# Kernel optimization log

Measured on AMD Instinct MI355X. Metric: run time of the kernel, lower is better.

## Reference

```python
import jax, jax.numpy as jnp
import numpy as np

N = 4096
IN_DIM = 256
OUT_DIM = 256
H = 4
D = OUT_DIM // H  # per-head dim (concat=True)
ALPHA = 0.2
NEG_INF = -9e15


def setup_inputs() -> dict:
    key = jax.random.key(0)
    k1, k2, k3, k4, k5 = jax.random.split(key, 5)
    h = jax.random.normal(k1, (N, IN_DIM), dtype=jnp.float32)
    adj = jax.random.randint(k2, (N, N), 0, 2, dtype=jnp.int32)
    # Linear params (torch Linear: y = x @ W.T + b), xavier_uniform gain=1.414
    lim_w = 1.414 * np.sqrt(6.0 / (IN_DIM + H * D))
    W = jax.random.uniform(k3, (H * D, IN_DIM), dtype=jnp.float32, minval=-lim_w, maxval=lim_w)
    b = jnp.zeros((H * D,), dtype=jnp.float32)
    lim_a = 1.414 * np.sqrt(6.0 / (H + 2 * D))
    a = jax.random.uniform(k4, (H, 2 * D), dtype=jnp.float32, minval=-lim_a, maxval=lim_a)
    return {"h": h, "adj": adj, "W": W, "b": b, "a": a}


def reference(h, adj, W, b, a):
    # Wh: [N, H, D]
    Wh = (h @ W.T + b).reshape(N, H, D)
    # e_ij = leakyrelu(a . [Wh_i ; Wh_j]) decomposed into src/dst parts
    src = jnp.einsum('nhd,hd->nh', Wh, a[:, :D])   # [N, H], contribution of node i
    dst = jnp.einsum('nhd,hd->nh', Wh, a[:, D:])   # [N, H], contribution of node j
    e = src[:, None, :] + dst[None, :, :]          # [N, N, H]
    e = jax.nn.leaky_relu(e, negative_slope=ALPHA)
    # dense mask: non-edges get -9e15 (matches the original fill)
    att = jnp.where(adj[:, :, None] == 1, e, NEG_INF)
    att = jax.nn.softmax(att, axis=1)              # softmax over neighbors j per row i
    # dropout skipped (eval mode / deterministic reference)
    h_prime = jnp.einsum('ijh,jhd->ihd', att, Wh)  # [N, H, D]
    return h_prime.reshape(N, H * D)               # concat=True
```

## Files before the change

### kernel.cpp

```cpp
#include <hip/hip_runtime.h>

#define NN 4096
#define ALPHA 0.2f
#define FLTMAX 3.402823466e+38f

typedef __attribute__((ext_vector_type(8))) short short8x;
typedef __attribute__((ext_vector_type(4))) float f32x4;
typedef __attribute__((ext_vector_type(4))) unsigned short ushort4x;
typedef unsigned long long u64;

__device__ __forceinline__ float lrelu(float x) { return x > 0.f ? x : ALPHA * x; }

__device__ __forceinline__ unsigned short f2bf(float f) {
  unsigned u = __float_as_uint(f);
  u += 0x7fffu + ((u >> 16) & 1u);
  return (unsigned short)(u >> 16);
}
__device__ __forceinline__ float bf2f(unsigned short s) {
  return __uint_as_float(((unsigned)s) << 16);
}
__device__ __forceinline__ unsigned fkey(float f) {
  unsigned b = __float_as_uint(f);
  return (b & 0x80000000u) ? ~b : (b | 0x80000000u);
}
__device__ __forceinline__ float funkey(unsigned k) {
  return __uint_as_float((k & 0x80000000u) ? (k & 0x7fffffffu) : ~k);
}

__global__ __launch_bounds__(256) void k0_prep(
    const float* __restrict__ W, unsigned short* __restrict__ Whi,
    unsigned short* __restrict__ Wlo, unsigned* __restrict__ dmaxkey)
{
  const int t = threadIdx.x;
  const int idx = blockIdx.x * 256 + t;
  float4 v = ((const float4*)W)[idx];
  const float vf[4] = {v.x, v.y, v.z, v.w};
  ushort4x hi, lo;
#pragma unroll
  for (int q = 0; q < 4; ++q) {
    unsigned short hb = f2bf(vf[q]);
    hi[q] = hb;
    lo[q] = f2bf(vf[q] - bf2f(hb));
  }
  ((ushort4x*)Whi)[idx] = hi;
  ((ushort4x*)Wlo)[idx] = lo;
  if (blockIdx.x == 0 && t < 4) dmaxkey[t] = 0x00800000u;
}

__global__ __launch_bounds__(256) void k1_mfma(
    const float* __restrict__ hin, const unsigned short* __restrict__ Whi,
    const unsigned short* __restrict__ Wlo, const float* __restrict__ bias,
    const float* __restrict__ av, unsigned short* __restrict__ WhT,
    float* __restrict__ srcv, float* __restrict__ dstv_soa,
    unsigned* __restrict__ dmaxkey)
{
  __shared__ float lds_s[4][16], lds_d[4][16];
  const int t = threadIdx.x;
  const int rb = blockIdx.x >> 2, h = blockIdx.x & 3;
  const int m0 = rb * 16;
  const int w = t >> 6, l = t & 63, r = l & 15, g = l >> 4;
  const int d = w * 16 + r;
  const int col = h * 64 + d;

  f32x4 acc = (f32x4){0.f, 0.f, 0.f, 0.f};
  const float* arow = hin + (size_t)(m0 + r) * 256 + g * 8;
  const unsigned short* bh = Whi + (size_t)col * 256 + g * 8;
  const unsigned short* bl = Wlo + (size_t)col * 256 + g * 8;

#pragma unroll
  for (int ks = 0; ks < 8; ++ks) {
    float4 a0 = *(const float4*)(arow + ks * 32);
    float4 a1 = *(const float4*)(arow + ks * 32 + 4);
    const float af[8] = {a0.x, a0.y, a0.z, a0.w, a1.x, a1.y, a1.z, a1.w};
    short8x ahi, alo;
#pragma unroll
    for (int j = 0; j < 8; ++j) {
      unsigned short hb = f2bf(af[j]);
      ahi[j] = (short)hb;
      alo[j] = (short)f2bf(af[j] - bf2f(hb));
    }
    short8x bhf = *(const short8x*)(bh + ks * 32);
    short8x blf = *(const short8x*)(bl + ks * 32);
    acc = __builtin_amdgcn_mfma_f32_16x16x32_bf16(ahi, bhf, acc, 0, 0, 0);
    acc = __builtin_amdgcn_mfma_f32_16x16x32_bf16(ahi, blf, acc, 0, 0, 0);
    acc = __builtin_amdgcn_mfma_f32_16x16x32_bf16(alo, bhf, acc, 0, 0, 0);
  }

  const float bc = bias[col];
  const float asrc = av[h * 128 + d];
  const float adst = av[h * 128 + 64 + d];
  float wv[4];
  ushort4x st;
#pragma unroll
  for (int q = 0; q < 4; ++q) {
    wv[q] = acc[q] + bc;
    st[q] = f2bf(wv[q]);
  }
  *(ushort4x*)(WhT + (size_t)col * NN + m0 + 4 * g) = st;

#pragma unroll
  for (int q = 0; q < 4; ++q) {
    float s = wv[q] * asrc, dd = wv[q] * adst;
#pragma unroll
    for (int off = 8; off >= 1; off >>= 1) {
      s += __shfl_xor(s, off);
      dd += __shfl_xor(dd, off);
    }
    if (r == 0) { lds_s[w][4 * g + q] = s; lds_d[w][4 * g + q] = dd; }
  }
  __syncthreads();
  if (t < 64) {
    const int row = t & 15;
    float s = lds_s[0][row] + lds_s[1][row] + lds_s[2][row] + lds_s[3][row];
    float dd = lds_d[0][row] + lds_d[1][row] + lds_d[2][row] + lds_d[3][row];
    if (t < 16) {
      srcv[(size_t)(m0 + row) * 4 + h] = s;
      dstv_soa[(size_t)h * NN + m0 + row] = dd;
    }
    float m = dd;
#pragma unroll
    for (int off = 1; off <= 32; off <<= 1) m = fmaxf(m, __shfl_xor(m, off));
    if (t == 0) atomicMax(dmaxkey + h, fkey(m));
  }
}

__global__ __launch_bounds__(256) void k2_mask(
    const int* __restrict__ adj, u64* __restrict__ bmask)
{
  const int t = threadIdx.x, wid = t >> 6, l = t & 63;
  const int row = blockIdx.x * 4 + wid;
  const int4* ap = (const int4*)(adj + (size_t)row * NN) + l;
  const int sh = 4 * (l & 15);
#pragma unroll
  for (int it = 0; it < 16; ++it) {
    int4 v = ap[(size_t)it * 64];
    unsigned nib = (v.x & 1) | ((v.y & 1) << 1) | ((v.z & 1) << 2) | ((v.w & 1) << 3);
    u64 w = (u64)nib << sh;
    w |= __shfl_xor(w, 1);
    w |= __shfl_xor(w, 2);
    w |= __shfl_xor(w, 4);
    w |= __shfl_xor(w, 8);
    if ((l & 15) == 0) bmask[(size_t)row * 64 + it * 4 + (l >> 4)] = w;
  }
}

__global__ __launch_bounds__(256) void k3_mfma(
    const unsigned short* __restrict__ WhT, const float* __restrict__ srcv,
    const float* __restrict__ dstv_soa, const unsigned* __restrict__ dmaxkey,
    const u64* __restrict__ bmask,
    float* __restrict__ pacc, float* __restrict__ pden)
{
  const int t = threadIdx.x;
  const int rb = blockIdx.x & 255, s = blockIdx.x >> 8;
  const int i0 = rb * 16;
  const int w0 = s * 16;
  const int h  = t >> 6;
  const int l  = t & 63;
  const int r  = l & 15;
  const int g  = l >> 4;

  const float dmax = funkey(dmaxkey[h]);
  const float sr0 = srcv[(size_t)(i0 + r) * 4 + h];
  const float mr0 = lrelu(sr0 + dmax);

  f32x4 acc[4];
#pragma unroll
  for (int n = 0; n < 4; ++n) acc[n] = (f32x4){0.f, 0.f, 0.f, 0.f};
  float dacc0 = 0.f;

  const unsigned short* whb = WhT + (size_t)(h * 64 + r) * NN + s * 1024 + g * 8;
  const float* dpb = dstv_soa + (size_t)h * NN + s * 1024 + g * 8;
  const u64* mb0 = bmask + (size_t)(i0 + r) * 64 + w0;

  for (int tile = 0; tile < 16; ++tile) {
    const u64 wm0 = mb0[tile];
#pragma unroll
    for (int kt = 0; kt < 2; ++kt) {
      float4 da = *(const float4*)(dpb + tile * 64 + kt * 32);
      float4 db = *(const float4*)(dpb + tile * 64 + kt * 32 + 4);
      const unsigned bits0 = (unsigned)(wm0 >> (kt * 32 + g * 8)) & 0xffu;
      const float dvs[8] = {da.x, da.y, da.z, da.w, db.x, db.y, db.z, db.w};
      short8x a0;
#pragma unroll
      for (int jj = 0; jj < 8; ++jj) {
        float e0 = lrelu(sr0 + dvs[jj]);
        float p0 = ((bits0 >> jj) & 1u) ? __expf(e0 - mr0) : 0.f;
        unsigned short pb0 = f2bf(p0);
        a0[jj] = (short)pb0;
        dacc0 += bf2f(pb0);
      }
      short8x bfr[4];
#pragma unroll
      for (int n = 0; n < 4; ++n)
        bfr[n] = *(const short8x*)(whb + (size_t)(n * 16) * NN + tile * 64 + kt * 32);
#pragma unroll
      for (int n = 0; n < 4; ++n)
        acc[n] = __builtin_amdgcn_mfma_f32_16x16x32_bf16(a0, bfr[n], acc[n], 0, 0, 0);
    }
  }

  dacc0 += __shfl_xor(dacc0, 16); dacc0 += __shfl_xor(dacc0, 32);
  if (l < 16) pden[((size_t)s * NN + i0 + l) * 4 + h] = dacc0;

#pragma unroll
  for (int n = 0; n < 4; ++n)
#pragma unroll
    for (int q = 0; q < 4; ++q)
      pacc[((size_t)s * NN + i0 + g * 4 + q) * 256 + h * 64 + n * 16 + r] = acc[n][q];
}

__global__ __launch_bounds__(256) void k4_combine(
    const float* __restrict__ pacc, const float* __restrict__ pden,
    float* __restrict__ out)
{
  const int t = threadIdx.x;
  const int i = blockIdx.x * 4 + (t >> 6);
  const int c4 = t & 63;
  const int h = c4 >> 4;
  const float4* pa = (const float4*)pacc;
  float4 num = {0.f, 0.f, 0.f, 0.f};
  float den = 0.f;
#pragma unroll
  for (int s = 0; s < 4; ++s) {
    float4 v = pa[((size_t)(s * NN + i)) * 64 + c4];
    num.x += v.x; num.y += v.y; num.z += v.z; num.w += v.w;
    den += pden[((size_t)s * NN + i) * 4 + h];
  }
  float inv = 1.f / den;
  float4 o = {num.x * inv, num.y * inv, num.z * inv, num.w * inv};
  ((float4*)out)[(size_t)i * 64 + c4] = o;
}

extern "C" void kernel_launch(void* const* d_in, const int* in_sizes, int n_in,
                              void* d_out, int out_size, void* d_ws, size_t ws_size,
                              hipStream_t stream) {
  const float* hin  = (const float*)d_in[0];
  const int*   adj  = (const int*)d_in[1];
  const float* W    = (const float*)d_in[2];
  const float* bias = (const float*)d_in[3];
  const float* av   = (const float*)d_in[4];
  float* out = (float*)d_out;

  char* ws = (char*)d_ws;
  unsigned short* WhT = (unsigned short*)(ws + 0x0);
  unsigned short* Whi = (unsigned short*)(ws + 0x200000);
  unsigned short* Wlo = (unsigned short*)(ws + 0x220000);
  float* srcv  = (float*)(ws + 0x240000);
  float* dstv  = (float*)(ws + 0x250000);
  unsigned* dmaxkey = (unsigned*)(ws + 0x260000);
  u64* bmask   = (u64*)(ws + 0x261000);
  float* pacc  = (float*)(ws + 0x461000);
  float* pden  = (float*)(ws + 0x1461000);

  k0_prep<<<64, 256, 0, stream>>>(W, Whi, Wlo, dmaxkey);
  k1_mfma<<<1024, 256, 0, stream>>>(hin, Whi, Wlo, bias, av, WhT, srcv, dstv, dmaxkey);
  k2_mask<<<1024, 256, 0, stream>>>(adj, bmask);
  k3_mfma<<<1024, 256, 0, stream>>>(WhT, srcv, dstv, dmaxkey, bmask, pacc, pden);
  k4_combine<<<NN / 4, 256, 0, stream>>>(pacc, pden, out);
}
```

Before: 212.4 us.

## Process two row tiles per wave sharing B fragments, split K across waves, use exp2

```diff
diff --git a/kernel.cpp b/kernel.cpp
--- a/kernel.cpp
+++ b/kernel.cpp
@@ -3,13 +3,12 @@
 #define NN 4096
 #define ALPHA 0.2f
 #define FLTMAX 3.402823466e+38f
+#define LOG2E 1.44269504088896340736f
 
 typedef __attribute__((ext_vector_type(8))) short short8x;
 typedef __attribute__((ext_vector_type(4))) float f32x4;
 typedef __attribute__((ext_vector_type(4))) unsigned short ushort4x;
 typedef unsigned long long u64;
-
-__device__ __forceinline__ float lrelu(float x) { return x > 0.f ? x : ALPHA * x; }
 
 __device__ __forceinline__ unsigned short f2bf(float f) {
   unsigned u = __float_as_uint(f);
@@ -106,7 +105,7 @@
       s += __shfl_xor(s, off);
       dd += __shfl_xor(dd, off);
     }
-    if (r == 0) { lds_s[w][4 * g + q] = s; lds_d[w][4 * g + q] = dd; }
+    if (r == 0) { lds_s[w][4 * g + q] = s * LOG2E; lds_d[w][4 * g + q] = dd * LOG2E; }
   }
   __syncthreads();
   if (t < 64) {
@@ -144,69 +143,118 @@
   }
 }
 
-__global__ __launch_bounds__(256) void k3_mfma(
+__global__ __launch_bounds__(256, 4) void k3_mfma(
     const unsigned short* __restrict__ WhT, const float* __restrict__ srcv,
     const float* __restrict__ dstv_soa, const unsigned* __restrict__ dmaxkey,
     const u64* __restrict__ bmask,
     float* __restrict__ pacc, float* __restrict__ pden)
 {
+  __shared__ float lds_acc[2][64][33];
+  __shared__ float lds_den[2][64][2];
   const int t = threadIdx.x;
-  const int rb = blockIdx.x & 255, s = blockIdx.x >> 8;
-  const int i0 = rb * 16;
-  const int w0 = s * 16;
-  const int h  = t >> 6;
-  const int l  = t & 63;
-  const int r  = l & 15;
-  const int g  = l >> 4;
+  const int c  = blockIdx.x & 7;
+  const int s  = c >> 1, hp = c & 1;
+  const int rb = blockIdx.x >> 3;
+  const int i0 = rb * 32;
+  const int w = t >> 6, l = t & 63;
+  const int hsel = w & 1, jh = w >> 1;
+  const int h = hp * 2 + hsel;
+  const int r = l & 15, g = l >> 4;
+  const int j0 = s * 1024 + jh * 512;
 
   const float dmax = funkey(dmaxkey[h]);
   const float sr0 = srcv[(size_t)(i0 + r) * 4 + h];
-  const float mr0 = lrelu(sr0 + dmax);
-
-  f32x4 acc[4];
-#pragma unroll
-  for (int n = 0; n < 4; ++n) acc[n] = (f32x4){0.f, 0.f, 0.f, 0.f};
-  float dacc0 = 0.f;
-
-  const unsigned short* whb = WhT + (size_t)(h * 64 + r) * NN + s * 1024 + g * 8;
-  const float* dpb = dstv_soa + (size_t)h * NN + s * 1024 + g * 8;
-  const u64* mb0 = bmask + (size_t)(i0 + r) * 64 + w0;
-
-  for (int tile = 0; tile < 16; ++tile) {
+  const float sr1 = srcv[(size_t)(i0 + 16 + r) * 4 + h];
+  const float x0m = sr0 + dmax, x1m = sr1 + dmax;
+  const float mr0 = fmaxf(x0m, ALPHA * x0m);
+  const float mr1 = fmaxf(x1m, ALPHA * x1m);
+
+  f32x4 acc[2][4];
+#pragma unroll
+  for (int m = 0; m < 2; ++m)
+#pragma unroll
+    for (int n = 0; n < 4; ++n) acc[m][n] = (f32x4){0.f, 0.f, 0.f, 0.f};
+  float dacc0 = 0.f, dacc1 = 0.f;
+
+  const unsigned short* whb = WhT + (size_t)(h * 64 + r) * NN + j0 + g * 8;
+  const float* dpb = dstv_soa + (size_t)h * NN + j0 + g * 8;
+  const u64* mb0 = bmask + (size_t)(i0 + r) * 64 + s * 16 + jh * 8;
+  const u64* mb1 = bmask + (size_t)(i0 + 16 + r) * 64 + s * 16 + jh * 8;
+
+  for (int tile = 0; tile < 8; ++tile) {
     const u64 wm0 = mb0[tile];
+    const u64 wm1 = mb1[tile];
 #pragma unroll
     for (int kt = 0; kt < 2; ++kt) {
       float4 da = *(const float4*)(dpb + tile * 64 + kt * 32);
       float4 db = *(const float4*)(dpb + tile * 64 + kt * 32 + 4);
       const unsigned bits0 = (unsigned)(wm0 >> (kt * 32 + g * 8)) & 0xffu;
+      const unsigned bits1 = (unsigned)(wm1 >> (kt * 32 + g * 8)) & 0xffu;
       const float dvs[8] = {da.x, da.y, da.z, da.w, db.x, db.y, db.z, db.w};
-      short8x a0;
+      short8x a0, a1;
 #pragma unroll
       for (int jj = 0; jj < 8; ++jj) {
-        float e0 = lrelu(sr0 + dvs[jj]);
-        float p0 = ((bits0 >> jj) & 1u) ? __expf(e0 - mr0) : 0.f;
-        unsigned short pb0 = f2bf(p0);
-        a0[jj] = (short)pb0;
-        dacc0 += bf2f(pb0);
+        float x0 = sr0 + dvs[jj];
+        float e0 = fmaxf(x0, ALPHA * x0) - mr0;
+        e0 = ((bits0 >> jj) & 1u) ? e0 : -200.0f;
+        unsigned pu0 = __float_as_uint(exp2f(e0));
+        dacc0 += __uint_as_float(pu0 & 0xffff0000u);
+        a0[jj] = (short)(pu0 >> 16);
+        float x1 = sr1 + dvs[jj];
+        float e1 = fmaxf(x1, ALPHA * x1) - mr1;
+        e1 = ((bits1 >> jj) & 1u) ? e1 : -200.0f;
+        unsigned pu1 = __float_as_uint(exp2f(e1));
+        dacc1 += __uint_as_float(pu1 & 0xffff0000u);
+        a1[jj] = (short)(pu1 >> 16);
       }
       short8x bfr[4];
 #pragma unroll
       for (int n = 0; n < 4; ++n)
         bfr[n] = *(const short8x*)(whb + (size_t)(n * 16) * NN + tile * 64 + kt * 32);
 #pragma unroll
+      for (int n = 0; n < 4; ++n) {
+        acc[0][n] = __builtin_amdgcn_mfma_f32_16x16x32_bf16(a0, bfr[n], acc[0][n], 0, 0, 0);
+        acc[1][n] = __builtin_amdgcn_mfma_f32_16x16x32_bf16(a1, bfr[n], acc[1][n], 0, 0, 0);
+      }
+    }
+  }
+
+  if (jh == 1) {
+#pragma unroll
+    for (int m = 0; m < 2; ++m)
+#pragma unroll
       for (int n = 0; n < 4; ++n)
-        acc[n] = __builtin_amdgcn_mfma_f32_16x16x32_bf16(a0, bfr[n], acc[n], 0, 0, 0);
-    }
-  }
-
-  dacc0 += __shfl_xor(dacc0, 16); dacc0 += __shfl_xor(dacc0, 32);
-  if (l < 16) pden[((size_t)s * NN + i0 + l) * 4 + h] = dacc0;
-
-#pragma unroll
-  for (int n = 0; n < 4; ++n)
-#pragma unroll
-    for (int q = 0; q < 4; ++q)
-      pacc[((size_t)s * NN + i0 + g * 4 + q) * 256 + h * 64 + n * 16 + r] = acc[n][q];
+#pragma unroll
+        for (int q = 0; q < 4; ++q)
+          lds_acc[hsel][l][m * 16 + n * 4 + q] = acc[m][n][q];
+    lds_den[hsel][l][0] = dacc0;
+    lds_den[hsel][l][1] = dacc1;
+  }
+  __syncthreads();
+  if (jh == 0) {
+#pragma unroll
+    for (int m = 0; m < 2; ++m)
+#pragma unroll
+      for (int n = 0; n < 4; ++n)
+#pragma unroll
+        for (int q = 0; q < 4; ++q)
+          acc[m][n][q] += lds_acc[hsel][l][m * 16 + n * 4 + q];
+    dacc0 += lds_den[hsel][l][0];
+    dacc1 += lds_den[hsel][l][1];
+    dacc0 += __shfl_xor(dacc0, 16); dacc0 += __shfl_xor(dacc0, 32);
+    dacc1 += __shfl_xor(dacc1, 16); dacc1 += __shfl_xor(dacc1, 32);
+    if (l < 16) {
+      pden[((size_t)s * NN + i0 + l) * 4 + h] = dacc0;
+      pden[((size_t)s * NN + i0 + 16 + l) * 4 + h] = dacc1;
+    }
+#pragma unroll
+    for (int m = 0; m < 2; ++m)
+#pragma unroll
+      for (int n = 0; n < 4; ++n)
+#pragma unroll
+        for (int q = 0; q < 4; ++q)
+          pacc[((size_t)s * NN + i0 + 16 * m + g * 4 + q) * 256 + h * 64 + n * 16 + r] = acc[m][n][q];
+  }
 }
 
 __global__ __launch_bounds__(256) void k4_combine(
```

After: 184.9 us. 12.9% less time.
